# Kernel optimization log

Measured on AMD Instinct MI355X. Metric: run time of the kernel, lower is better.

The kernel has to match this reference:

```python
import jax, jax.numpy as jnp
import numpy as np

N = 100000   # nodes
E = 25000    # hyperedges
NNZ = 2000000
IN_CH = 64
HEADS = 8
OUT_CH = 8
HO = HEADS * OUT_CH  # 64


def setup_inputs() -> dict:
    key = jax.random.key(0)
    k1, k2, k3, k4, k5 = jax.random.split(key, 5)
    X = jax.random.normal(k1, (N, IN_CH), dtype=jnp.float32)
    vertex = jax.random.randint(k2, (NNZ,), 0, N, dtype=jnp.int64 if jax.config.jax_enable_x64 else jnp.int32)
    edges = jax.random.randint(k3, (NNZ,), 0, E, dtype=jnp.int64 if jax.config.jax_enable_x64 else jnp.int32)
    homo = jax.random.uniform(k4, (E,), dtype=jnp.float32) + 0.1  # positive per-hyperedge scalar
    # nn.Linear(in, heads*out, bias=False): store as [in, heads*out] for X @ W
    W = jax.random.normal(k5, (IN_CH, HO), dtype=jnp.float32) * (1.0 / np.sqrt(IN_CH))
    return {"X": X, "W": W, "homo": homo, "vertex": vertex, "edges": edges}


def reference(X, W, homo, vertex, edges):
    n = X.shape[0]
    e = homo.shape[0]
    Xp = X @ W                                   # [N, H*O]
    Xve = Xp[vertex]                             # [nnz, H*O] gather node->incidence
    # first_aggregate = 'mean': vertex features -> hyperedge features
    Xe_sum = jax.ops.segment_sum(Xve, edges, num_segments=e)
    cnt = jax.ops.segment_sum(jnp.ones((Xve.shape[0],), Xve.dtype), edges, num_segments=e)
    Xe = Xe_sum / jnp.maximum(cnt, 1.0)[:, None]  # [E, H*O]
    Xev = Xe[edges]                              # [nnz, H*O] gather edge->incidence
    he = homo[edges]                             # [nnz]
    att_sum = jax.ops.segment_sum(he, vertex, num_segments=n)[vertex]  # [nnz]
    att = he / att_sum                           # [nnz] (homo > 0 so sums > 0 at incident slots)
    att_Xev = att[:, None] * Xev                 # fused version of att.mm(ones).mul(Xev)
    # second_aggregate = 'sum': hyperedge features -> node features
    Xv = jax.ops.segment_sum(att_Xev, vertex, num_segments=n)  # [N, H*O]
    out = Xp + Xv
    # use_norm: row-l2 normalize with DETACHED norm (scale is a constant wrt grad)
    rownorm = jax.lax.stop_gradient(jnp.linalg.norm(out, axis=1, keepdims=True))
    scale = jnp.where(rownorm > 0, 1.0 / jnp.maximum(rownorm, 1e-30), 0.0)
    return out * scale
```

## Files before the change

kernel.cpp:

```cpp
#include <hip/hip_runtime.h>
#include <hip/hip_bf16.h>


#define SE_LOG 7
#define SV_LOG 9
#define MAXB   2048
#define CH     16384

__device__ __forceinline__ float bf2f(unsigned short u) {
    union { unsigned int i; float f; } x;
    x.i = ((unsigned int)u) << 16;
    return x.f;
}

__device__ __forceinline__ float bflo(unsigned int u) {
    union { unsigned int i; float f; } x;
    x.i = u << 16;
    return x.f;
}

__device__ __forceinline__ float bfhi(unsigned int u) {
    union { unsigned int i; float f; } x;
    x.i = u & 0xffff0000u;
    return x.f;
}

__device__ __forceinline__ unsigned short f2bf(float f) {
    union { unsigned int i; float ff; } x;
    x.ff = f;
    unsigned int r = x.i + 0x7fff + ((x.i >> 16) & 1);
    return (unsigned short)(r >> 16);
}

__device__ __forceinline__ float loadF(const void* p, size_t i, int bf16mode) {
    return bf16mode ? bf2f(((const unsigned short*)p)[i]) : ((const float*)p)[i];
}

__device__ __forceinline__ int loadI(const void* p, size_t i, int i64mode) {
    return i64mode ? ((const int*)p)[2 * i] : ((const int*)p)[i];
}

__global__ void sniff_kernel(const void* X, const void* vtx, int* flags) {
    if (threadIdx.x != 0 || blockIdx.x != 0) return;
    const unsigned short* u = (const unsigned short*)X;
    int sane = 0;
    for (int i = 0; i < 64; ++i) {
        unsigned short lo = u[2 * i];
        int e = (lo >> 7) & 0xFF;
        if (e >= 110 && e <= 137) ++sane;
    }
    flags[0] = (sane >= 32) ? 1 : 0;
    const int* w = (const int*)vtx;
    int zeros = 0;
    for (int i = 0; i < 64; ++i)
        if (w[2 * i + 1] == 0) ++zeros;
    flags[1] = (zeros >= 32) ? 1 : 0;
}

__global__ void homof_kernel(const void* __restrict__ homo,
                             const int* __restrict__ flags,
                             float* __restrict__ homof, int E) {
    int i = blockIdx.x * blockDim.x + threadIdx.x;
    if (i < E) homof[i] = loadF(homo, i, flags[0]);
}

__global__ __launch_bounds__(256)
void gemm_kernel(const void* __restrict__ X, const void* __restrict__ W,
                 const int* __restrict__ flags,
                 unsigned short* __restrict__ Xpb, int N) {
    __shared__ float Ws[64 * 64];
    __shared__ float Xs[16][64];
    const int bmode = flags[0];
    int tid = threadIdx.x;
    for (int j = tid; j < 4096; j += 256) Ws[j] = loadF(W, j, bmode);
    __syncthreads();
    int lane = tid & 63, w = tid >> 6;
    int wid = (blockIdx.x * 256 + tid) >> 6;
    int nw  = (gridDim.x * 256) >> 6;
    for (int r0 = wid * 4; r0 < N; r0 += nw * 4) {
        if (r0 + 4 <= N) {
            float acc0 = 0.f, acc1 = 0.f, acc2 = 0.f, acc3 = 0.f;
#pragma unroll
            for (int j = 0; j < 4; ++j)
                Xs[w * 4 + j][lane] = loadF(X, (size_t)(r0 + j) * 64 + lane, bmode);
#pragma unroll
            for (int k4 = 0; k4 < 16; ++k4) {
                float4 x0 = *(const float4*)&Xs[w * 4 + 0][k4 * 4];
                float4 x1 = *(const float4*)&Xs[w * 4 + 1][k4 * 4];
                float4 x2 = *(const float4*)&Xs[w * 4 + 2][k4 * 4];
                float4 x3 = *(const float4*)&Xs[w * 4 + 3][k4 * 4];
#pragma unroll
                for (int kk = 0; kk < 4; ++kk) {
                    float wv = Ws[(k4 * 4 + kk) * 64 + lane];
                    acc0 = fmaf((&x0.x)[kk], wv, acc0);
                    acc1 = fmaf((&x1.x)[kk], wv, acc1);
                    acc2 = fmaf((&x2.x)[kk], wv, acc2);
                    acc3 = fmaf((&x3.x)[kk], wv, acc3);
                }
            }
            float a[4] = {acc0, acc1, acc2, acc3};
#pragma unroll
            for (int j = 0; j < 4; ++j)
                Xpb[(size_t)(r0 + j) * 64 + lane] = f2bf(a[j]);
        } else {
            for (int r = r0; r < N; ++r) {
                Xs[w * 4][lane] = loadF(X, (size_t)r * 64 + lane, bmode);
                float acc = 0.f;
                for (int k = 0; k < 64; ++k)
                    acc = fmaf(Xs[w * 4][k], Ws[k * 64 + lane], acc);
                Xpb[(size_t)r * 64 + lane] = f2bf(acc);
            }
        }
    }
}

__global__ __launch_bounds__(1024)
void bhist_kernel(const void* __restrict__ edges, const void* __restrict__ vertex,
                  const int* __restrict__ flags, int* __restrict__ btot,
                  int* __restrict__ slabc, int sstride,
                  int nnz, int NBE, int NBV, int GC) {
    __shared__ int cnt[MAXB];
    int blk  = blockIdx.x;
    int side = (blk >= GC) ? 1 : 0;
    int b    = side ? blk - GC : blk;
    const void* keys = side ? vertex : edges;
    int sblog = side ? SV_LOG : SE_LOG;
    int nb    = side ? NBV : NBE;
    int bas   = side ? NBE : 0;
    int tid = threadIdx.x;
    for (int j = tid; j < nb; j += 1024) cnt[j] = 0;
    __syncthreads();
    int imode = flags[1];
    int c0 = b * CH, c1 = min(nnz, c0 + CH);
    for (int i = c0 + tid; i < c1; i += 1024)
        atomicAdd(&cnt[loadI(keys, i, imode) >> sblog], 1);
    __syncthreads();
    for (int j = tid; j < nb; j += 1024) {
        int c = cnt[j];
        slabc[(size_t)blk * sstride + j] = c;
        if (c) atomicAdd(&btot[bas + j], c);
    }
}

__global__ void bscan_kernel(const int* __restrict__ btot, int* __restrict__ bbase,
                             int* __restrict__ bcur, int NBT) {
    __shared__ int wsum[16];
    __shared__ int carry_s;
    int tid = threadIdx.x, lane = tid & 63, w = tid >> 6;
    if (tid == 0) carry_s = 0;
    __syncthreads();
    for (int base = 0; base < NBT; base += 1024) {
        int i = base + tid;
        int x = (i < NBT) ? btot[i] : 0;
        int s = x;
#pragma unroll
        for (int d = 1; d < 64; d <<= 1) {
            int t = __shfl_up(s, d, 64);
            if (lane >= d) s += t;
        }
        if (lane == 63) wsum[w] = s;
        __syncthreads();
        if (w == 0 && lane < 16) {
            int v = wsum[lane];
#pragma unroll
            for (int d = 1; d < 16; d <<= 1) {
                int t = __shfl_up(v, d, 64);
                if (lane >= d) v += t;
            }
            wsum[lane] = v;
        }
        __syncthreads();
        int carry = carry_s;
        int excl  = carry + (w > 0 ? wsum[w - 1] : 0) + s - x;
        if (i < NBT) { bbase[i] = excl; bcur[i] = excl; }
        __syncthreads();
        if (tid == 1023) carry_s = carry + wsum[15];
        __syncthreads();
    }
    if (tid == 0) bbase[NBT] = carry_s;
}

__global__ __launch_bounds__(1024)
void bscatter_kernel(const void* __restrict__ edges, const void* __restrict__ vertex,
                     const int* __restrict__ flags, int* __restrict__ bcur,
                     const int* __restrict__ slabc, int sstride,
                     int* __restrict__ buck, int nnz, int NBE, int NBV, int GC,
                     int bitsN, int bitsE) {
    __shared__ int cnt[MAXB];
    __shared__ int gb[MAXB];
    int blk  = blockIdx.x;
    int side = (blk >= GC) ? 1 : 0;
    int b    = side ? blk - GC : blk;
    const void* keys = side ? vertex : edges;
    const void* pay  = side ? edges  : vertex;
    int sblog = side ? SV_LOG : SE_LOG;
    int psh   = side ? bitsE : bitsN;
    int nb    = side ? NBV : NBE;
    int bas   = side ? NBE : 0;
    int tid = threadIdx.x;
    for (int j = tid; j < nb; j += 1024) {
        int c = slabc[(size_t)blk * sstride + j];
        gb[j]  = c ? atomicAdd(&bcur[bas + j], c) : 0;
        cnt[j] = 0;
    }
    __syncthreads();
    int imode = flags[1];
    int c0 = b * CH, c1 = min(nnz, c0 + CH);
    int lmask = (1 << sblog) - 1;
    for (int i = c0 + tid; i < c1; i += 1024) {
        int k   = loadI(keys, i, imode);
        int bkt = k >> sblog;
        int r   = atomicAdd(&cnt[bkt], 1);
        buck[gb[bkt] + r] = ((k & lmask) << psh) | loadI(pay, i, imode);
    }
}

__global__ __launch_bounds__(1024)
void bfinal_kernel(const int* __restrict__ buck, const int* __restrict__ bbase,
                   const float* __restrict__ homof,
                   int* __restrict__ off, int* __restrict__ dest,
                   float* __restrict__ hs,
                   int NBE, int NBV, int E, int N, int bitsN, int bitsE) {
    __shared__ int cnt[1 << SV_LOG];
    __shared__ int sexc[1 << SV_LOG];
    __shared__ float hsum[1 << SV_LOG];
    __shared__ int wsum[16];
    int g    = blockIdx.x;
    int side = (g >= NBE) ? 1 : 0;
    int b    = side ? g - NBE : g;
    int sblog = side ? SV_LOG : SE_LOG;
    int psh   = side ? bitsE : bitsN;
    int pmask = (1 << psh) - 1;
    int nside = side ? N : E;
    int bin0  = b << sblog;
    int nbins = min(1 << sblog, nside - bin0);
    int goff0 = (side ? E : 0) + bin0;
    int s0 = bbase[g], s1 = bbase[g + 1], size = s1 - s0;
    int tid = threadIdx.x, lane = tid & 63, w = tid >> 6;
    for (int j = tid; j < nbins; j += 1024) { cnt[j] = 0; hsum[j] = 0.f; }
    __syncthreads();
    for (int j = tid; j < size; j += 1024)
        atomicAdd(&cnt[buck[s0 + j] >> psh], 1);
    __syncthreads();
    {
        int x = (tid < nbins) ? cnt[tid] : 0;
        int s = x;
#pragma unroll
        for (int d = 1; d < 64; d <<= 1) {
            int t = __shfl_up(s, d, 64);
            if (lane >= d) s += t;
        }
        if (lane == 63) wsum[w] = s;
        __syncthreads();
        if (w == 0 && lane < 16) {
            int v = wsum[lane];
#pragma unroll
            for (int d = 1; d < 16; d <<= 1) {
                int t = __shfl_up(v, d, 64);
                if (lane >= d) v += t;
            }
            wsum[lane] = v;
        }
        __syncthreads();
        int excl = s - x + (w > 0 ? wsum[w - 1] : 0);
        if (tid < nbins) { sexc[tid] = excl; off[goff0 + tid] = s0 + excl; }
    }
    if (side == 1 && b == NBV - 1 && tid == 0) off[E + N] = s1;
    __syncthreads();
    for (int j = tid; j < nbins; j += 1024) cnt[j] = sexc[j];
    __syncthreads();
    if (side == 1) {
        for (int j = tid; j < size; j += 1024) {
            int p  = buck[s0 + j];
            int lb = p >> psh;
            int r  = atomicAdd(&cnt[lb], 1);
            int e  = p & pmask;
            dest[s0 + r] = e;
            atomicAdd(&hsum[lb], homof[e]);
        }
        __syncthreads();
        for (int j = tid; j < nbins; j += 1024) hs[bin0 + j] = hsum[j];
    } else {
        for (int j = tid; j < size; j += 1024) {
            int p = buck[s0 + j];
            int r = atomicAdd(&cnt[p >> psh], 1);
            dest[s0 + r] = p & pmask;
        }
    }
}

__global__ void hist_atomic_kernel(const void* __restrict__ edges,
                                   const void* __restrict__ vertex,
                                   const int* __restrict__ flags,
                                   int* __restrict__ tot, int E, int nnz) {
    int i = blockIdx.x * blockDim.x + threadIdx.x;
    if (i >= nnz) return;
    int imode = flags[1];
    atomicAdd(&tot[loadI(edges, i, imode)], 1);
    atomicAdd(&tot[E + loadI(vertex, i, imode)], 1);
}

__global__ void scan_part_kernel(const int* __restrict__ tot, int* __restrict__ part, int M) {
    int g = blockIdx.x, tid = threadIdx.x;
    int base = g * 2048;
    int sum = 0;
    for (int j = tid; j < 2048; j += 256) {
        int i = base + j;
        sum += (i < M) ? tot[i] : 0;
    }
#pragma unroll
    for (int d = 32; d >= 1; d >>= 1) sum += __shfl_xor(sum, d, 64);
    __shared__ int wsums[4];
    int lane = tid & 63, w = tid >> 6;
    if (lane == 0) wsums[w] = sum;
    __syncthreads();
    if (tid == 0) part[g] = wsums[0] + wsums[1] + wsums[2] + wsums[3];
}

__global__ void scan_root_kernel(int* __restrict__ part, int G,
                                 int* __restrict__ off, int M) {
    int tid = threadIdx.x, lane = tid & 63, w = tid >> 6;
    int x = (tid < G) ? part[tid] : 0;
    int s = x;
#pragma unroll
    for (int d = 1; d < 64; d <<= 1) {
        int t = __shfl_up(s, d, 64);
        if (lane >= d) s += t;
    }
    __shared__ int ws[16];
    if (lane == 63) ws[w] = s;
    __syncthreads();
    if (w == 0 && lane < 16) {
        int v = ws[lane];
#pragma unroll
        for (int d = 1; d < 16; d <<= 1) {
            int t = __shfl_up(v, d, 64);
            if (lane >= d) v += t;
        }
        ws[lane] = v;
    }
    __syncthreads();
    int excl = s - x + (w > 0 ? ws[w - 1] : 0);
    if (tid < G) part[tid] = excl;
    if (tid == 1023) off[M] = ws[15];
}

__global__ void scan_apply_kernel(int* __restrict__ tot, const int* __restrict__ part,
                                  int* __restrict__ off, int M) {
    int g = blockIdx.x, tid = threadIdx.x, lane = tid & 63, w = tid >> 6;
    int base = g * 2048 + tid * 8;
    int e[8]; int s = 0;
#pragma unroll
    for (int j = 0; j < 8; ++j) {
        int i = base + j;
        e[j] = (i < M) ? tot[i] : 0;
        s += e[j];
    }
    int si = s;
#pragma unroll
    for (int d = 1; d < 64; d <<= 1) {
        int t = __shfl_up(si, d, 64);
        if (lane >= d) si += t;
    }
    __shared__ int wsum[4];
    if (lane == 63) wsum[w] = si;
    __syncthreads();
    int wbase = 0;
    for (int ww = 0; ww < w; ++ww) wbase += wsum[ww];
    int run = part[g] + wbase + si - s;
#pragma unroll
    for (int j = 0; j < 8; ++j) {
        int i = base + j;
        if (i < M) off[i] = run;
        run += e[j];
    }
}

__global__ void copy_kernel(const int* __restrict__ src, int* __restrict__ dst, int n) {
    int i = blockIdx.x * blockDim.x + threadIdx.x;
    if (i < n) dst[i] = src[i];
}

__global__ void scatter_atomic_kernel(const void* __restrict__ edges,
                                      const void* __restrict__ vertex,
                                      const int* __restrict__ flags,
                                      int* __restrict__ cur, int* __restrict__ dest,
                                      int E, int nnz) {
    int i = blockIdx.x * blockDim.x + threadIdx.x;
    if (i >= nnz) return;
    int imode = flags[1];
    int e = loadI(edges, i, imode);
    int v = loadI(vertex, i, imode);
    dest[atomicAdd(&cur[e], 1)]     = v;
    dest[atomicAdd(&cur[E + v], 1)] = e;
}

__global__ void hs_fallback_kernel(const int* __restrict__ off,
                                   const int* __restrict__ sorted,
                                   const float* __restrict__ homof,
                                   float* __restrict__ hs, int E, int N) {
    int v = blockIdx.x * blockDim.x + threadIdx.x;
    if (v >= N) return;
    int s = off[E + v], e = off[E + v + 1];
    float t = 0.f;
    for (int j = s; j < e; ++j) t += homof[sorted[j]];
    hs[v] = t;
}

__global__ void edge_mean_kernel(const unsigned short* __restrict__ Xpb,
                                 const int* __restrict__ off,
                                 const int* __restrict__ sorted,
                                 const float* __restrict__ homof,
                                 unsigned short* __restrict__ Ye, int E) {
    int wid  = (blockIdx.x * blockDim.x + threadIdx.x) >> 6;
    int lane = threadIdx.x & 63;
    if (wid >= E) return;
    int g = lane >> 4, c = lane & 15;
    unsigned co = (unsigned)c << 3;
    int start = off[wid], end = off[wid + 1];
    float a0 = 0.f, a1 = 0.f, a2 = 0.f, a3 = 0.f;
    const char* Xb = (const char*)Xpb;
    int j = start + g;
    for (; j + 12 < end; j += 16) {
        int v0 = sorted[j];
        int v1 = sorted[j + 4];
        int v2 = sorted[j + 8];
        int v3 = sorted[j + 12];
        uint2 u0 = *(const uint2*)(Xb + (((unsigned)v0 << 7) + co));
        uint2 u1 = *(const uint2*)(Xb + (((unsigned)v1 << 7) + co));
        uint2 u2 = *(const uint2*)(Xb + (((unsigned)v2 << 7) + co));
        uint2 u3 = *(const uint2*)(Xb + (((unsigned)v3 << 7) + co));
        a0 += (bflo(u0.x) + bflo(u1.x)) + (bflo(u2.x) + bflo(u3.x));
        a1 += (bfhi(u0.x) + bfhi(u1.x)) + (bfhi(u2.x) + bfhi(u3.x));
        a2 += (bflo(u0.y) + bflo(u1.y)) + (bflo(u2.y) + bflo(u3.y));
        a3 += (bfhi(u0.y) + bfhi(u1.y)) + (bfhi(u2.y) + bfhi(u3.y));
    }
    for (; j < end; j += 4) {
        int v = sorted[j];
        uint2 u = *(const uint2*)(Xb + (((unsigned)v << 7) + co));
        a0 += bflo(u.x); a1 += bfhi(u.x);
        a2 += bflo(u.y); a3 += bfhi(u.y);
    }
    a0 += __shfl_xor(a0, 16, 64); a0 += __shfl_xor(a0, 32, 64);
    a1 += __shfl_xor(a1, 16, 64); a1 += __shfl_xor(a1, 32, 64);
    a2 += __shfl_xor(a2, 16, 64); a2 += __shfl_xor(a2, 32, 64);
    a3 += __shfl_xor(a3, 16, 64); a3 += __shfl_xor(a3, 32, 64);
    if (g == 0) {
        float inv = homof[wid] / fmaxf((float)(end - start), 1.f);
        unsigned p0 = (unsigned)f2bf(a0 * inv) | ((unsigned)f2bf(a1 * inv) << 16);
        unsigned p1 = (unsigned)f2bf(a2 * inv) | ((unsigned)f2bf(a3 * inv) << 16);
        *(uint2*)((char*)Ye + (((unsigned)wid << 7) + co)) = make_uint2(p0, p1);
    }
}

__global__ void vertex_out_kernel(const unsigned short* __restrict__ Xpb,
                                  const unsigned short* __restrict__ Ye,
                                  const int* __restrict__ off,
                                  const int* __restrict__ sorted,
                                  const float* __restrict__ hs,
                                  float* __restrict__ out, int E, int N) {
    int wid  = (blockIdx.x * blockDim.x + threadIdx.x) >> 6;
    int lane = threadIdx.x & 63;
    if (wid >= N) return;
    int g = lane >> 4, c = lane & 15;
    unsigned co = (unsigned)c << 3;
    int start = off[E + wid], end = off[E + wid + 1];
    float a0 = 0.f, a1 = 0.f, a2 = 0.f, a3 = 0.f;
    const char* Xb = (const char*)Ye;
    int j = start + g;
    for (; j + 12 < end; j += 16) {
        int e0 = sorted[j];
        int e1 = sorted[j + 4];
        int e2 = sorted[j + 8];
        int e3 = sorted[j + 12];
        uint2 u0 = *(const uint2*)(Xb + (((unsigned)e0 << 7) + co));
        uint2 u1 = *(const uint2*)(Xb + (((unsigned)e1 << 7) + co));
        uint2 u2 = *(const uint2*)(Xb + (((unsigned)e2 << 7) + co));
        uint2 u3 = *(const uint2*)(Xb + (((unsigned)e3 << 7) + co));
        a0 += (bflo(u0.x) + bflo(u1.x)) + (bflo(u2.x) + bflo(u3.x));
        a1 += (bfhi(u0.x) + bfhi(u1.x)) + (bfhi(u2.x) + bfhi(u3.x));
        a2 += (bflo(u0.y) + bflo(u1.y)) + (bflo(u2.y) + bflo(u3.y));
        a3 += (bfhi(u0.y) + bfhi(u1.y)) + (bfhi(u2.y) + bfhi(u3.y));
    }
    for (; j < end; j += 4) {
        int e = sorted[j];
        uint2 u = *(const uint2*)(Xb + (((unsigned)e << 7) + co));
        a0 += bflo(u.x); a1 += bfhi(u.x);
        a2 += bflo(u.y); a3 += bfhi(u.y);
    }
    a0 += __shfl_xor(a0, 16, 64); a0 += __shfl_xor(a0, 32, 64);
    a1 += __shfl_xor(a1, 16, 64); a1 += __shfl_xor(a1, 32, 64);
    a2 += __shfl_xor(a2, 16, 64); a2 += __shfl_xor(a2, 32, 64);
    a3 += __shfl_xor(a3, 16, 64); a3 += __shfl_xor(a3, 32, 64);
    if (g == 0) {
        float hsv = hs[wid];
        float inv = (hsv > 0.f) ? 1.f / hsv : 0.f;
        uint2 xu = *(const uint2*)((const char*)Xpb + (((unsigned)wid << 7) + co));
        float r0 = bflo(xu.x) + a0 * inv, r1 = bfhi(xu.x) + a1 * inv;
        float r2 = bflo(xu.y) + a2 * inv, r3 = bfhi(xu.y) + a3 * inv;
        float ss = r0 * r0 + r1 * r1 + r2 * r2 + r3 * r3;
        ss += __shfl_xor(ss, 1, 64); ss += __shfl_xor(ss, 2, 64);
        ss += __shfl_xor(ss, 4, 64); ss += __shfl_xor(ss, 8, 64);
        float rn    = sqrtf(ss);
        float scale = (rn > 0.f) ? 1.f / fmaxf(rn, 1e-30f) : 0.f;
        float4 o = make_float4(r0 * scale, r1 * scale, r2 * scale, r3 * scale);
        *(float4*)((char*)out + (((unsigned)wid << 8) + (co << 1))) = o;
    }
}

static inline int ceil_bits(int n) {
    int v = n - 1;
    if (v < 1) v = 1;
    int b = 0;
    while ((1 << b) <= v) ++b;
    return b;
}

extern "C" void kernel_launch(void* const* d_in, const int* in_sizes, int n_in,
                              void* d_out, int out_size, void* d_ws, size_t ws_size,
                              hipStream_t stream) {
    const void* X      = d_in[0];
    const void* W      = d_in[1];
    const void* homo   = d_in[2];
    const void* vertex = d_in[3];
    const void* edges  = d_in[4];
    float* out = (float*)d_out;

    const int N   = in_sizes[0] / 64;
    const int E   = in_sizes[2];
    const int NNZ = in_sizes[3];
    const int M   = E + N;

    const int NBE = (E + (1 << SE_LOG) - 1) >> SE_LOG;
    const int NBV = (N + (1 << SV_LOG) - 1) >> SV_LOG;
    const int NBT = NBE + NBV;
    const int GC  = (NNZ + CH - 1) / CH;
    const int SST = (NBE > NBV ? NBE : NBV);
    const int bitsN = ceil_bits(N);
    const int bitsE = ceil_bits(E);
    const int G   = (M + 2047) / 2048;

    char*  ws = (char*)d_ws;
    size_t o  = 0;
    auto alloc = [&](size_t bytes) -> void* {
        void* p = ws + o;
        o += (bytes + 255) & ~(size_t)255;
        return p;
    };
    int*            flags = (int*)alloc(2 * 4);
    int*            off   = (int*)alloc((size_t)(M + 1) * 4);
    int*            bbase = (int*)alloc((size_t)(NBT + 1) * 4);
    int*            bcur  = (int*)alloc((size_t)NBT * 4);
    int*            btot  = (int*)alloc((size_t)NBT * 4);
    float*          homof = (float*)alloc((size_t)E * 4);
    float*          hs    = (float*)alloc((size_t)N * 4);
    int*            buck  = (int*)alloc((size_t)2 * NNZ * 4);
    int*            sorted= (int*)alloc((size_t)2 * NNZ * 4);
    unsigned short* Xpb   = (unsigned short*)alloc((size_t)N * 64 * 2);
    unsigned short* Ye    = (unsigned short*)alloc((size_t)E * 64 * 2);
    int*            slabc = (int*)alloc((size_t)2 * GC * SST * 4);
    size_t o_common = o;
    bool fast = (o <= ws_size) && NBE <= MAXB && NBV <= MAXB &&
                (SE_LOG + bitsN <= 32) && (SV_LOG + bitsE <= 32) && G <= 1024;
    (void)n_in; (void)out_size;

    sniff_kernel<<<1, 64, 0, stream>>>(X, vertex, flags);
    homof_kernel<<<(E + 255) / 256, 256, 0, stream>>>(homo, flags, homof, E);
    gemm_kernel<<<512, 256, 0, stream>>>(X, W, flags, Xpb, N);

    if (fast) {
        hipMemsetAsync(btot, 0, (size_t)NBT * 4, stream);
        bhist_kernel<<<2 * GC, 1024, 0, stream>>>(edges, vertex, flags, btot,
                                                  slabc, SST, NNZ, NBE, NBV, GC);
        bscan_kernel<<<1, 1024, 0, stream>>>(btot, bbase, bcur, NBT);
        bscatter_kernel<<<2 * GC, 1024, 0, stream>>>(edges, vertex, flags, bcur,
                                                     slabc, SST, buck, NNZ,
                                                     NBE, NBV, GC, bitsN, bitsE);
        bfinal_kernel<<<NBT, 1024, 0, stream>>>(buck, bbase, homof, off, sorted,
                                                hs, NBE, NBV, E, N, bitsN, bitsE);
    } else {
        o = o_common;
        int* tot  = (int*)alloc((size_t)M * 4);
        int* part = (int*)alloc((size_t)(G + 1) * 4);
        int* cur  = (int*)alloc((size_t)M * 4);
        hipMemsetAsync(tot, 0, (size_t)M * 4, stream);
        int nb = (NNZ + 255) / 256;
        hist_atomic_kernel<<<nb, 256, 0, stream>>>(edges, vertex, flags, tot, E, NNZ);
        scan_part_kernel<<<G, 256, 0, stream>>>(tot, part, M);
        scan_root_kernel<<<1, 1024, 0, stream>>>(part, G, off, M);
        scan_apply_kernel<<<G, 256, 0, stream>>>(tot, part, off, M);
        copy_kernel<<<(M + 255) / 256, 256, 0, stream>>>(off, cur, M);
        scatter_atomic_kernel<<<nb, 256, 0, stream>>>(edges, vertex, flags, cur, sorted, E, NNZ);
        hs_fallback_kernel<<<(N + 255) / 256, 256, 0, stream>>>(off, sorted, homof, hs, E, N);
    }

    edge_mean_kernel<<<(E + 3) / 4, 256, 0, stream>>>(Xpb, off, sorted, homof, Ye, E);
    vertex_out_kernel<<<(N + 3) / 4, 256, 0, stream>>>(Xpb, Ye, off, sorted,
                                                       hs, out, E, N);
}
```

Baseline: 280.2 us.

## Map eight vertices per wave in vertex_out and shrink sort bucket sizes

The vertex output kernel now gives each vertex 8 lanes instead of a full 64-lane wave. Each lane loads 16-byte uint4 chunks and reduces serially over that vertex's incident edges, which removes the cross-group shuffle reduction and the idle lanes at the write-out. With about 20 incidences per vertex, the old layout split work across 4 groups and then wasted 48 lanes on the final step. Separately, the SE_LOG/SV_LOG/CH sizing constants are halved, changing bucket and chunk sizes in the sort and partition stage. The risk is longer serial gather chains per lane and divergence when neighbouring vertices have different degrees.

Measured after the change: 264.8 us. -5.5%, faster.

```diff
diff --git a/kernel.cpp b/kernel.cpp
--- a/kernel.cpp
+++ b/kernel.cpp
@@ -2,10 +2,10 @@
 #include <hip/hip_bf16.h>
 
 
-#define SE_LOG 7
-#define SV_LOG 9
+#define SE_LOG 6
+#define SV_LOG 8
 #define MAXB   2048
-#define CH     16384
+#define CH     8192
 
 __device__ __forceinline__ float bf2f(unsigned short u) {
     union { unsigned int i; float f; } x;
@@ -459,53 +459,57 @@
                                   const int* __restrict__ sorted,
                                   const float* __restrict__ hs,
                                   float* __restrict__ out, int E, int N) {
-    int wid  = (blockIdx.x * blockDim.x + threadIdx.x) >> 6;
+    int wv   = (blockIdx.x * blockDim.x + threadIdx.x) >> 6;
     int lane = threadIdx.x & 63;
-    if (wid >= N) return;
-    int g = lane >> 4, c = lane & 15;
-    unsigned co = (unsigned)c << 3;
-    int start = off[E + wid], end = off[E + wid + 1];
+    int g = lane >> 3, c = lane & 7;
+    int vid = wv * 8 + g;
+    if (vid >= N) return;
+    unsigned co = (unsigned)c << 4;
+    int start = off[E + vid], end = off[E + vid + 1];
     float a0 = 0.f, a1 = 0.f, a2 = 0.f, a3 = 0.f;
-    const char* Xb = (const char*)Ye;
-    int j = start + g;
-    for (; j + 12 < end; j += 16) {
-        int e0 = sorted[j];
-        int e1 = sorted[j + 4];
-        int e2 = sorted[j + 8];
-        int e3 = sorted[j + 12];
-        uint2 u0 = *(const uint2*)(Xb + (((unsigned)e0 << 7) + co));
-        uint2 u1 = *(const uint2*)(Xb + (((unsigned)e1 << 7) + co));
-        uint2 u2 = *(const uint2*)(Xb + (((unsigned)e2 << 7) + co));
-        uint2 u3 = *(const uint2*)(Xb + (((unsigned)e3 << 7) + co));
+    float a4 = 0.f, a5 = 0.f, a6 = 0.f, a7 = 0.f;
+    const char* Yb = (const char*)Ye;
+    int j = start;
+    for (; j + 3 < end; j += 4) {
+        int e0 = sorted[j], e1 = sorted[j + 1], e2 = sorted[j + 2], e3 = sorted[j + 3];
+        uint4 u0 = *(const uint4*)(Yb + (((unsigned)e0 << 7) + co));
+        uint4 u1 = *(const uint4*)(Yb + (((unsigned)e1 << 7) + co));
+        uint4 u2 = *(const uint4*)(Yb + (((unsigned)e2 << 7) + co));
+        uint4 u3 = *(const uint4*)(Yb + (((unsigned)e3 << 7) + co));
         a0 += (bflo(u0.x) + bflo(u1.x)) + (bflo(u2.x) + bflo(u3.x));
         a1 += (bfhi(u0.x) + bfhi(u1.x)) + (bfhi(u2.x) + bfhi(u3.x));
         a2 += (bflo(u0.y) + bflo(u1.y)) + (bflo(u2.y) + bflo(u3.y));
         a3 += (bfhi(u0.y) + bfhi(u1.y)) + (bfhi(u2.y) + bfhi(u3.y));
-    }
-    for (; j < end; j += 4) {
+        a4 += (bflo(u0.z) + bflo(u1.z)) + (bflo(u2.z) + bflo(u3.z));
+        a5 += (bfhi(u0.z) + bfhi(u1.z)) + (bfhi(u2.z) + bfhi(u3.z));
+        a6 += (bflo(u0.w) + bflo(u1.w)) + (bflo(u2.w) + bflo(u3.w));
+        a7 += (bfhi(u0.w) + bfhi(u1.w)) + (bfhi(u2.w) + bfhi(u3.w));
+    }
+    for (; j < end; ++j) {
         int e = sorted[j];
-        uint2 u = *(const uint2*)(Xb + (((unsigned)e << 7) + co));
+        uint4 u = *(const uint4*)(Yb + (((unsigned)e << 7) + co));
         a0 += bflo(u.x); a1 += bfhi(u.x);
         a2 += bflo(u.y); a3 += bfhi(u.y);
-    }
-    a0 += __shfl_xor(a0, 16, 64); a0 += __shfl_xor(a0, 32, 64);
-    a1 += __shfl_xor(a1, 16, 64); a1 += __shfl_xor(a1, 32, 64);
-    a2 += __shfl_xor(a2, 16, 64); a2 += __shfl_xor(a2, 32, 64);
-    a3 += __shfl_xor(a3, 16, 64); a3 += __shfl_xor(a3, 32, 64);
-    if (g == 0) {
-        float hsv = hs[wid];
-        float inv = (hsv > 0.f) ? 1.f / hsv : 0.f;
-        uint2 xu = *(const uint2*)((const char*)Xpb + (((unsigned)wid << 7) + co));
-        float r0 = bflo(xu.x) + a0 * inv, r1 = bfhi(xu.x) + a1 * inv;
-        float r2 = bflo(xu.y) + a2 * inv, r3 = bfhi(xu.y) + a3 * inv;
-        float ss = r0 * r0 + r1 * r1 + r2 * r2 + r3 * r3;
-        ss += __shfl_xor(ss, 1, 64); ss += __shfl_xor(ss, 2, 64);
-        ss += __shfl_xor(ss, 4, 64); ss += __shfl_xor(ss, 8, 64);
-        float rn    = sqrtf(ss);
-        float scale = (rn > 0.f) ? 1.f / fmaxf(rn, 1e-30f) : 0.f;
-        float4 o = make_float4(r0 * scale, r1 * scale, r2 * scale, r3 * scale);
-        *(float4*)((char*)out + (((unsigned)wid << 8) + (co << 1))) = o;
-    }
+        a4 += bflo(u.z); a5 += bfhi(u.z);
+        a6 += bflo(u.w); a7 += bfhi(u.w);
+    }
+    float hsv = hs[vid];
+    float inv = (hsv > 0.f) ? 1.f / hsv : 0.f;
+    uint4 xu = *(const uint4*)((const char*)Xpb + (((unsigned)vid << 7) + co));
+    float r0 = bflo(xu.x) + a0 * inv, r1 = bfhi(xu.x) + a1 * inv;
+    float r2 = bflo(xu.y) + a2 * inv, r3 = bfhi(xu.y) + a3 * inv;
+    float r4 = bflo(xu.z) + a4 * inv, r5 = bfhi(xu.z) + a5 * inv;
+    float r6 = bflo(xu.w) + a6 * inv, r7 = bfhi(xu.w) + a7 * inv;
+    float ss = ((r0 * r0 + r1 * r1) + (r2 * r2 + r3 * r3)) +
+               ((r4 * r4 + r5 * r5) + (r6 * r6 + r7 * r7));
+    ss += __shfl_xor(ss, 1, 64);
+    ss += __shfl_xor(ss, 2, 64);
+    ss += __shfl_xor(ss, 4, 64);
+    float rn    = sqrtf(ss);
+    float scale = (rn > 0.f) ? 1.f / fmaxf(rn, 1e-30f) : 0.f;
+    char* ob = (char*)out + (((unsigned)vid << 8) + (co << 1));
+    *(float4*)ob        = make_float4(r0 * scale, r1 * scale, r2 * scale, r3 * scale);
+    *(float4*)(ob + 16) = make_float4(r4 * scale, r5 * scale, r6 * scale, r7 * scale);
 }
 
 static inline int ceil_bits(int n) {
@@ -595,6 +599,8 @@
     }
 
     edge_mean_kernel<<<(E + 3) / 4, 256, 0, stream>>>(Xpb, off, sorted, homof, Ye, E);
-    vertex_out_kernel<<<(N + 3) / 4, 256, 0, stream>>>(Xpb, Ye, off, sorted,
-                                                       hs, out, E, N);
-}
+    int vwaves  = (N + 7) / 8;
+    int vblocks = (vwaves * 64 + 255) / 256;
+    vertex_out_kernel<<<vblocks, 256, 0, stream>>>(Xpb, Ye, off, sorted,
+                                                   hs, out, E, N);
+}
```
